# Performance work log

Hardware: AMD Instinct MI355X
Metric: run time of the kernel (lower is better)

The kernel has to match this reference:

```python
import jax, jax.numpy as jnp
import numpy as np

N = 8192
D = 256
DENSITY = 0.02  # ~164 neighbors per node


def setup_inputs() -> dict:
    key = jax.random.key(0)
    k1, k2, k3, k4 = jax.random.split(key, 4)
    inputs = jax.random.normal(k1, (N, D), dtype=jnp.float32)
    vals = jax.random.uniform(k2, (N, N), dtype=jnp.float32, minval=0.1, maxval=1.0)
    mask = jax.random.uniform(k3, (N, N), dtype=jnp.float32) < DENSITY
    adj = jnp.where(mask, vals, 0.0)
    H_v = 0.1 * jax.random.normal(k4, (D, 1), dtype=jnp.float32)
    return {"inputs": inputs, "adj": adj, "H_v": H_v}


def reference(inputs, adj, H_v):
    # scores[j] = inputs[j] . H_v  -> sparse values v_ij = adj_ij * scores[j]
    scores = jnp.squeeze(inputs @ H_v, -1)            # [N]
    mask = adj != 0.0                                  # nonzero pattern of SparseTensor
    logits = adj * scores[None, :]                     # [N, N]
    neg = jnp.asarray(jnp.finfo(logits.dtype).min, logits.dtype)
    logits = jnp.where(mask, logits, neg)
    # sparse softmax: normalize only over nonzero entries per row
    m = jnp.max(logits, axis=1, keepdims=True)
    e = jnp.where(mask, jnp.exp(logits - m), 0.0)
    s = jnp.sum(e, axis=1, keepdims=True)
    weights = e / jnp.where(s > 0, s, 1.0)             # empty rows -> all-zero weights
    # sparse_tensor_dense_matmul(weights, inputs)
    return weights @ inputs                            # [N, D]
```

## Files before the change

### kernel.cpp

```cpp
#include <hip/hip_runtime.h>

#define NN 8192
#define DD 256
#define RT 32
#define KC 128
#define KS 2
#define KRANGE (NN / KS)
#define NCH (KRANGE / KC)

typedef float v4f __attribute__((ext_vector_type(4)));
typedef short short8 __attribute__((ext_vector_type(8)));
typedef float f32x4 __attribute__((ext_vector_type(4)));
typedef unsigned short u16x4 __attribute__((ext_vector_type(4)));
typedef unsigned short u16x8 __attribute__((ext_vector_type(8)));

__device__ __forceinline__ unsigned short f2bf_rne(float x) {
    unsigned u = __float_as_uint(x);
    u += 0x7fffu + ((u >> 16) & 1u);
    return (unsigned short)(u >> 16);
}
__device__ __forceinline__ float bf_to_f(unsigned short b) {
    return __uint_as_float((unsigned)b << 16);
}

__global__ __launch_bounds__(256) void scores_kernel(const float* __restrict__ inputs,
                                                     const float* __restrict__ Hv,
                                                     float* __restrict__ scores) {
    int wave = threadIdx.x >> 6;
    int lane = threadIdx.x & 63;
    int row  = blockIdx.x * 4 + wave;
    if (row >= NN) return;
    float4 v = ((const float4*)(inputs + (size_t)row * DD))[lane];
    float4 h = ((const float4*)Hv)[lane];
    float s = v.x * h.x + v.y * h.y + v.z * h.z + v.w * h.w;
    #pragma unroll
    for (int off = 32; off > 0; off >>= 1) s += __shfl_down(s, off, 64);
    if (lane == 0) scores[row] = s;
}

#define XP 258
__global__ __launch_bounds__(256) void xtp_kernel(const float* __restrict__ inputs,
                                                  unsigned short* __restrict__ xtp) {
    __shared__ unsigned short sx[64 * XP];
    const int tid = threadIdx.x;
    const int k0  = blockIdx.x * 64;
    #pragma unroll
    for (int r = 0; r < 16; ++r) {
        int row = r * 4 + (tid >> 6);
        int col = (tid & 63) * 4;
        float4 v = *(const float4*)(inputs + (size_t)(k0 + row) * DD + col);
        u16x4 w;
        w[0] = f2bf_rne(v.x); w[1] = f2bf_rne(v.y); w[2] = f2bf_rne(v.z); w[3] = f2bf_rne(v.w);
        *(u16x4*)&sx[row * XP + col] = w;
    }
    __syncthreads();
    #pragma unroll
    for (int r = 0; r < 8; ++r) {
        int rid  = r * 256 + tid;
        int lane = rid & 63;
        int t    = (rid >> 6) & 15;
        int kcl  = rid >> 10;
        int n    = t * 16 + (lane & 15);
        int kl   = kcl * 32 + (lane >> 4) * 8;
        u16x8 w;
        #pragma unroll
        for (int j = 0; j < 8; ++j) w[j] = sx[(kl + j) * XP + n];
        size_t kcg = (size_t)(k0 >> 5) + kcl;
        *(u16x8*)(xtp + (((size_t)t * 256 + kcg) * 64 + lane) * 8) = w;
    }
}

__global__ __launch_bounds__(512, 4) void spmm_kernel(const float* __restrict__ adj,
                                                      const unsigned short* __restrict__ xtp,
                                                      const float* __restrict__ scores,
                                                      float* __restrict__ pc,
                                                      float* __restrict__ pd) {
    __shared__ unsigned short sE[2][RT * KC];
    const int tid  = threadIdx.x;
    const int lane = tid & 63;
    const int wave = tid >> 6;
    const int q    = lane >> 4;
    const int m16  = lane & 15;

    const int ks   = blockIdx.x & (KS - 1);
    const int mb   = blockIdx.x >> 1;
    const int row0 = mb * RT;
    const int kbase = ks * KRANGE;

    const int lrow = tid >> 4;
    const int kgb  = tid & 15;
    const int kg   = kgb * 8;
    const float* arow = adj + (size_t)(row0 + lrow) * NN + kbase;

    f32x4 acc[2][2] = {};
    float den = 0.f;

    v4f a0 = __builtin_nontemporal_load((const v4f*)(arow + kg));
    v4f a1 = __builtin_nontemporal_load((const v4f*)(arow + kg + 4));
    float4 s0 = *(const float4*)(scores + kbase + kg);
    float4 s1 = *(const float4*)(scores + kbase + kg + 4);

    for (int c = 0; c < NCH; ++c) {
        const int cn = (c + 1 < NCH ? c + 1 : c) * KC;
        v4f na0 = __builtin_nontemporal_load((const v4f*)(arow + cn + kg));
        v4f na1 = __builtin_nontemporal_load((const v4f*)(arow + cn + kg + 4));
        float4 ns0 = *(const float4*)(scores + kbase + cn + kg);
        float4 ns1 = *(const float4*)(scores + kbase + cn + kg + 4);

        float af[8] = { a0.x, a0.y, a0.z, a0.w, a1.x, a1.y, a1.z, a1.w };
        float sf[8] = { s0.x, s0.y, s0.z, s0.w, s1.x, s1.y, s1.z, s1.w };
        u16x8 ev;
        #pragma unroll
        for (int i = 0; i < 8; ++i) {
            float e = (af[i] != 0.f) ? __expf(af[i] * sf[i]) : 0.f;
            unsigned short b = f2bf_rne(e);
            ev[i] = b;
            den += bf_to_f(b);
        }
        *(u16x8*)&sE[c & 1][lrow * KC + ((kgb ^ (lrow & 15)) * 8)] = ev;
        __syncthreads();

        const size_t kcg0 = (size_t)((kbase + c * KC) >> 5);
        short8 bfr[2][4];
        #pragma unroll
        for (int nt = 0; nt < 2; ++nt) {
            const size_t t = (size_t)(wave * 2 + nt);
            #pragma unroll
            for (int kh = 0; kh < 4; ++kh)
                bfr[nt][kh] = *(const short8*)(xtp + ((t * 256 + kcg0 + kh) * 64 + lane) * 8);
        }
        const unsigned short* Eb = sE[c & 1];
        short8 afr[2][4];
        #pragma unroll
        for (int mt = 0; mt < 2; ++mt)
            #pragma unroll
            for (int kh = 0; kh < 4; ++kh)
                afr[mt][kh] = *(const short8*)&Eb[(mt * 16 + m16) * KC + (((kh * 4 + q) ^ m16) * 8)];

        #pragma unroll
        for (int mt = 0; mt < 2; ++mt)
            #pragma unroll
            for (int nt = 0; nt < 2; ++nt)
                #pragma unroll
                for (int kh = 0; kh < 4; ++kh)
                    acc[mt][nt] = __builtin_amdgcn_mfma_f32_16x16x32_bf16(
                        afr[mt][kh], bfr[nt][kh], acc[mt][nt], 0, 0, 0);

        a0 = na0; a1 = na1; s0 = ns0; s1 = ns1;
    }

    #pragma unroll
    for (int d = 1; d < 16; d <<= 1) den += __shfl_xor(den, d, 64);
    if ((tid & 15) == 0) pd[(size_t)ks * NN + row0 + lrow] = den;

    float* pcb = pc + ((size_t)ks * NN + row0) * DD;
    #pragma unroll
    for (int mt = 0; mt < 2; ++mt)
        #pragma unroll
        for (int nt = 0; nt < 2; ++nt)
            #pragma unroll
            for (int r = 0; r < 4; ++r) {
                int rr = mt * 16 + q * 4 + r;
                pcb[(size_t)rr * DD + wave * 32 + nt * 16 + m16] = acc[mt][nt][r];
            }
}

__global__ __launch_bounds__(256) void reduce_kernel(const float* __restrict__ pc,
                                                     const float* __restrict__ pd,
                                                     float* __restrict__ out) {
    const int row = blockIdx.x;
    const int tid = threadIdx.x;
    float d = pd[row] + pd[NN + row];
    float v = pc[(size_t)row * DD + tid] + pc[((size_t)NN + row) * DD + tid];
    out[(size_t)row * DD + tid] = (d > 0.f) ? v / d : 0.f;
}

__global__ __launch_bounds__(256) void attn_fallback(const float* __restrict__ adj,
                                                     const float* __restrict__ inputs,
                                                     const float* __restrict__ scores,
                                                     float* __restrict__ out) {
    __shared__ int   s_j[1024];
    __shared__ float s_e[1024];
    __shared__ int   s_cnt;
    const int row = blockIdx.x;
    const int tid = threadIdx.x;
    const float* arow = adj + (size_t)row * NN;
    float acc = 0.f, ssum = 0.f;
    for (int base = 0; base < NN; base += 1024) {
        if (tid == 0) s_cnt = 0;
        __syncthreads();
        float4 a = ((const float4*)(arow + base))[tid];
        int j0 = base + tid * 4;
        if (a.x != 0.f) { int k = atomicAdd(&s_cnt, 1); s_j[k] = j0 + 0; s_e[k] = __expf(a.x * scores[j0 + 0]); }
        if (a.y != 0.f) { int k = atomicAdd(&s_cnt, 1); s_j[k] = j0 + 1; s_e[k] = __expf(a.y * scores[j0 + 1]); }
        if (a.z != 0.f) { int k = atomicAdd(&s_cnt, 1); s_j[k] = j0 + 2; s_e[k] = __expf(a.z * scores[j0 + 2]); }
        if (a.w != 0.f) { int k = atomicAdd(&s_cnt, 1); s_j[k] = j0 + 3; s_e[k] = __expf(a.w * scores[j0 + 3]); }
        __syncthreads();
        int c = s_cnt;
        for (int k = 0; k < c; ++k) {
            float e = s_e[k];
            acc  += e * inputs[(size_t)s_j[k] * DD + tid];
            ssum += e;
        }
        __syncthreads();
    }
    out[(size_t)row * DD + tid] = (ssum > 0.f) ? acc / ssum : 0.f;
}

extern "C" void kernel_launch(void* const* d_in, const int* in_sizes, int n_in,
                              void* d_out, int out_size, void* d_ws, size_t ws_size,
                              hipStream_t stream) {
    const float* inputs = (const float*)d_in[0];
    const float* adj    = (const float*)d_in[1];
    const float* Hv     = (const float*)d_in[2];
    float* out = (float*)d_out;

    char* ws = (char*)d_ws;
    float*          scores = (float*)ws;
    unsigned short* xtp    = (unsigned short*)(ws + 32768);
    float*          pd     = (float*)(ws + 32768 + (size_t)NN * DD * 2);
    float*          pc     = (float*)(ws + 32768 + (size_t)NN * DD * 2 + KS * NN * 4);

    const size_t need = 32768 + (size_t)NN * DD * 2 + (size_t)KS * NN * 4
                      + (size_t)KS * NN * DD * 4;

    scores_kernel<<<NN / 4, 256, 0, stream>>>(inputs, Hv, scores);
    if (ws_size >= need) {
        xtp_kernel<<<NN / 64, 256, 0, stream>>>(inputs, xtp);
        spmm_kernel<<<(NN / RT) * KS, 512, 0, stream>>>(adj, xtp, scores, pc, pd);
        reduce_kernel<<<NN, 256, 0, stream>>>(pc, pd, out);
    } else {
        attn_fallback<<<NN, 256, 0, stream>>>(adj, inputs, scores, out);
    }
}
```

Before: 399.5 us.

## Split K four ways, stage scores in LDS, prefetch adjacency two chunks ahead

Raises the K-split from 2 to 4, which doubles the grid to more blocks of shorter K ranges and makes the reduce kernel sum four partials. Each block now copies its slice of scores into shared memory once instead of reloading them per chunk. Adjacency loads are double-buffered two chunks ahead, and the A fragments are read from LDS inside the MFMA loop to lower register pressure. The extra partial buffers add global traffic and reduce-kernel work, and the added LDS could affect occupancy.

```diff
diff --git a/kernel.cpp b/kernel.cpp
--- a/kernel.cpp
+++ b/kernel.cpp
@@ -4,7 +4,7 @@
 #define DD 256
 #define RT 32
 #define KC 128
-#define KS 2
+#define KS 4
 #define KRANGE (NN / KS)
 #define NCH (KRANGE / KC)
 
@@ -76,16 +76,20 @@
                                                       float* __restrict__ pc,
                                                       float* __restrict__ pd) {
     __shared__ unsigned short sE[2][RT * KC];
+    __shared__ float sS[KRANGE];
+
     const int tid  = threadIdx.x;
     const int lane = tid & 63;
     const int wave = tid >> 6;
     const int q    = lane >> 4;
     const int m16  = lane & 15;
 
-    const int ks   = blockIdx.x & (KS - 1);
-    const int mb   = blockIdx.x >> 1;
-    const int row0 = mb * RT;
+    const int ks    = blockIdx.x & (KS - 1);
+    const int mb    = blockIdx.x >> 2;
+    const int row0  = mb * RT;
     const int kbase = ks * KRANGE;
+
+    ((float4*)sS)[tid] = ((const float4*)(scores + kbase))[tid];
 
     const int lrow = tid >> 4;
     const int kgb  = tid & 15;
@@ -95,30 +99,16 @@
     f32x4 acc[2][2] = {};
     float den = 0.f;
 
-    v4f a0 = __builtin_nontemporal_load((const v4f*)(arow + kg));
-    v4f a1 = __builtin_nontemporal_load((const v4f*)(arow + kg + 4));
-    float4 s0 = *(const float4*)(scores + kbase + kg);
-    float4 s1 = *(const float4*)(scores + kbase + kg + 4);
+    v4f pa[2][2];
+    pa[0][0] = __builtin_nontemporal_load((const v4f*)(arow + kg));
+    pa[0][1] = __builtin_nontemporal_load((const v4f*)(arow + kg + 4));
+    pa[1][0] = __builtin_nontemporal_load((const v4f*)(arow + KC + kg));
+    pa[1][1] = __builtin_nontemporal_load((const v4f*)(arow + KC + kg + 4));
+
+    __syncthreads();
 
     for (int c = 0; c < NCH; ++c) {
-        const int cn = (c + 1 < NCH ? c + 1 : c) * KC;
-        v4f na0 = __builtin_nontemporal_load((const v4f*)(arow + cn + kg));
-        v4f na1 = __builtin_nontemporal_load((const v4f*)(arow + cn + kg + 4));
-        float4 ns0 = *(const float4*)(scores + kbase + cn + kg);
-        float4 ns1 = *(const float4*)(scores + kbase + cn + kg + 4);
-
-        float af[8] = { a0.x, a0.y, a0.z, a0.w, a1.x, a1.y, a1.z, a1.w };
-        float sf[8] = { s0.x, s0.y, s0.z, s0.w, s1.x, s1.y, s1.z, s1.w };
-        u16x8 ev;
-        #pragma unroll
-        for (int i = 0; i < 8; ++i) {
-            float e = (af[i] != 0.f) ? __expf(af[i] * sf[i]) : 0.f;
-            unsigned short b = f2bf_rne(e);
-            ev[i] = b;
-            den += bf_to_f(b);
-        }
-        *(u16x8*)&sE[c & 1][lrow * KC + ((kgb ^ (lrow & 15)) * 8)] = ev;
-        __syncthreads();
+        const int s = c & 1;
 
         const size_t kcg0 = (size_t)((kbase + c * KC) >> 5);
         short8 bfr[2][4];
@@ -129,24 +119,37 @@
             for (int kh = 0; kh < 4; ++kh)
                 bfr[nt][kh] = *(const short8*)(xtp + ((t * 256 + kcg0 + kh) * 64 + lane) * 8);
         }
-        const unsigned short* Eb = sE[c & 1];
-        short8 afr[2][4];
-        #pragma unroll
-        for (int mt = 0; mt < 2; ++mt)
-            #pragma unroll
-            for (int kh = 0; kh < 4; ++kh)
-                afr[mt][kh] = *(const short8*)&Eb[(mt * 16 + m16) * KC + (((kh * 4 + q) ^ m16) * 8)];
-
-        #pragma unroll
-        for (int mt = 0; mt < 2; ++mt)
-            #pragma unroll
-            for (int nt = 0; nt < 2; ++nt)
-                #pragma unroll
-                for (int kh = 0; kh < 4; ++kh)
-                    acc[mt][nt] = __builtin_amdgcn_mfma_f32_16x16x32_bf16(
-                        afr[mt][kh], bfr[nt][kh], acc[mt][nt], 0, 0, 0);
-
-        a0 = na0; a1 = na1; s0 = ns0; s1 = ns1;
+
+        float af[8] = { pa[s][0].x, pa[s][0].y, pa[s][0].z, pa[s][0].w,
+                        pa[s][1].x, pa[s][1].y, pa[s][1].z, pa[s][1].w };
+        u16x8 ev;
+        #pragma unroll
+        for (int i = 0; i < 8; ++i) {
+            float a = af[i];
+            float e = (a != 0.f) ? __expf(a * sS[c * KC + kg + i]) : 0.f;
+            unsigned short b = f2bf_rne(e);
+            ev[i] = b;
+            den += bf_to_f(b);
+        }
+
+        if (c + 2 < NCH) {
+            pa[s][0] = __builtin_nontemporal_load((const v4f*)(arow + (c + 2) * KC + kg));
+            pa[s][1] = __builtin_nontemporal_load((const v4f*)(arow + (c + 2) * KC + kg + 4));
+        }
+
+        *(u16x8*)&sE[s][lrow * KC + ((kgb ^ (lrow & 15)) * 8)] = ev;
+        __syncthreads();
+
+        const unsigned short* Eb = sE[s];
+        #pragma unroll
+        for (int kh = 0; kh < 4; ++kh) {
+            short8 a0 = *(const short8*)&Eb[m16 * KC + (((kh * 4 + q) ^ m16) * 8)];
+            short8 a1 = *(const short8*)&Eb[(16 + m16) * KC + (((kh * 4 + q) ^ m16) * 8)];
+            acc[0][0] = __builtin_amdgcn_mfma_f32_16x16x32_bf16(a0, bfr[0][kh], acc[0][0], 0, 0, 0);
+            acc[0][1] = __builtin_amdgcn_mfma_f32_16x16x32_bf16(a0, bfr[1][kh], acc[0][1], 0, 0, 0);
+            acc[1][0] = __builtin_amdgcn_mfma_f32_16x16x32_bf16(a1, bfr[0][kh], acc[1][0], 0, 0, 0);
+            acc[1][1] = __builtin_amdgcn_mfma_f32_16x16x32_bf16(a1, bfr[1][kh], acc[1][1], 0, 0, 0);
+        }
     }
 
     #pragma unroll
@@ -170,8 +173,12 @@
                                                      float* __restrict__ out) {
     const int row = blockIdx.x;
     const int tid = threadIdx.x;
-    float d = pd[row] + pd[NN + row];
-    float v = pc[(size_t)row * DD + tid] + pc[((size_t)NN + row) * DD + tid];
+    float d = 0.f, v = 0.f;
+    #pragma unroll
+    for (int ks = 0; ks < KS; ++ks) {
+        d += pd[(size_t)ks * NN + row];
+        v += pc[((size_t)ks * NN + row) * DD + tid];
+    }
     out[(size_t)row * DD + tid] = (d > 0.f) ? v / d : 0.f;
 }
 
```

Result: slower. 411.5 us (+3.0%).
